# Kernel tuning notes

Measured on AMD Instinct MI355X. Metric: run time of the kernel, lower is better.

## Reference

```python
import jax, jax.numpy as jnp
import numpy as np

N = 50000
E = 1600000
IN_C = 128
HID = 128
OUT_C = 64


def setup_inputs() -> dict:
    key = jax.random.key(0)
    ks = jax.random.split(key, 10)
    x = jax.random.normal(ks[0], (N, IN_C), dtype=jnp.float32)
    edge_index = jax.random.randint(ks[1], (2, E), 0, N, dtype=jnp.int64)
    s = lambda fan_in: 1.0 / np.sqrt(fan_in)
    W1 = jax.random.uniform(ks[2], (HID, IN_C), jnp.float32, -s(IN_C), s(IN_C))
    b1 = jnp.zeros((HID,), jnp.float32)
    Wc = jax.random.uniform(ks[3], (HID, HID + IN_C), jnp.float32, -s(HID + IN_C), s(HID + IN_C))
    bc = jax.random.uniform(ks[4], (HID,), jnp.float32, -s(HID + IN_C), s(HID + IN_C))
    W2 = jax.random.uniform(ks[5], (HID, HID), jnp.float32, -s(HID), s(HID))
    b2 = jnp.zeros((HID,), jnp.float32)
    Wo = jax.random.uniform(ks[6], (OUT_C, 2 * HID), jnp.float32, -s(2 * HID), s(2 * HID))
    bo = jax.random.uniform(ks[7], (OUT_C,), jnp.float32, -s(2 * HID), s(2 * HID))
    return {"x": x, "edge_index": edge_index, "W1": W1, "b1": b1,
            "Wc": Wc, "bc": bc, "W2": W2, "b2": b2, "Wo": Wo, "bo": bo}


def _gcn_conv(x, src, dst, norm, W, b):
    # PyG GCNConv: h = x @ W^T, propagate with sym-norm coeffs, add bias.
    h = x @ W.T                                   # [N, F_out]
    msg = h[src] * norm[:, None]                  # gather + scale, [E+N, F_out]
    out = jax.ops.segment_sum(msg, dst, num_segments=N)  # scatter-add
    return out + b


def _norm_coeffs(edge_index):
    # add self-loops, then sym normalization: D^{-1/2} A_hat D^{-1/2}
    loop = jnp.arange(N, dtype=edge_index.dtype)
    src = jnp.concatenate([edge_index[0], loop])
    dst = jnp.concatenate([edge_index[1], loop])
    deg = jax.ops.segment_sum(jnp.ones_like(dst, dtype=jnp.float32), dst, num_segments=N)
    dis = jnp.where(deg > 0, jax.lax.rsqrt(deg), 0.0)
    norm = dis[src] * dis[dst]
    return src, dst, norm


def reference(x, edge_index, W1, b1, Wc, bc, W2, b2, Wo, bo):
    src, dst, norm = _norm_coeffs(edge_index)
    x_agg = jax.nn.relu(_gcn_conv(x, src, dst, norm, W1, b1))
    x_comb = jnp.concatenate([x_agg, x], axis=1)
    x_comb = jax.nn.relu(x_comb @ Wc.T + bc)
    # dropout is identity in eval mode
    x_agg2 = _gcn_conv(x_comb, src, dst, norm, W2, b2)
    x_out = jnp.concatenate([x_agg2, x_comb], axis=1)
    return x_out @ Wo.T + bo
```

## Files before the change

kernel.cpp:

```cpp
#include <hip/hip_runtime.h>
#include <hip/hip_fp16.h>

#define Nn 50000
#define Ee 1600000
#define NPART 8

typedef __attribute__((ext_vector_type(8))) short short8;
typedef __attribute__((ext_vector_type(4))) float f32x4;
typedef unsigned short ushort;
typedef unsigned int uint;

__device__ __forceinline__ ushort f32_to_bf16(float f) {
    unsigned u = __builtin_bit_cast(unsigned, f);
    unsigned r = u + 0x7FFFu + ((u >> 16) & 1u);
    return (ushort)(r >> 16);
}
__device__ __forceinline__ float bf16_to_f32(ushort h) {
    unsigned u = ((unsigned)h) << 16;
    return __builtin_bit_cast(float, u);
}


__global__ void hist_rank_kernel(const int* __restrict__ dst, int* __restrict__ counts8,
                                 int* __restrict__ rank) {
    int e = blockIdx.x * blockDim.x + threadIdx.x;
    int p = blockIdx.x & (NPART - 1);
    if (e < Ee) rank[e] = atomicAdd(&counts8[p * Nn + dst[e]], 1);
}

__global__ void scan1_kernel(const int* __restrict__ counts8, int* __restrict__ offsets,
                             int* __restrict__ partials) {
    __shared__ int sd[256];
    int t = threadIdx.x;
    int i = blockIdx.x * 256 + t;
    int c = 0;
    if (i < Nn) {
        #pragma unroll
        for (int p = 0; p < NPART; ++p) c += counts8[p * Nn + i];
    }
    int v = c;
    #pragma unroll
    for (int off = 1; off < 256; off <<= 1) {
        sd[t] = v; __syncthreads();
        int add = (t >= off) ? sd[t - off] : 0;
        __syncthreads();
        v += add;
    }
    if (i < Nn) offsets[i] = v - c;
    if (t == 255) partials[blockIdx.x] = v;
}

__global__ void scan3_kernel(int* __restrict__ offsets, const int* __restrict__ partials,
                             const int* __restrict__ counts8, int* __restrict__ pbase8,
                             float* __restrict__ dis) {
    __shared__ int sd[256];
    int t = threadIdx.x;
    int s = (t < blockIdx.x) ? partials[t] : 0;
    sd[t] = s; __syncthreads();
    #pragma unroll
    for (int off = 128; off > 0; off >>= 1) {
        if (t < off) sd[t] += sd[t + off];
        __syncthreads();
    }
    int base = sd[0];
    int i = blockIdx.x * 256 + t;
    if (i == 0) offsets[Nn] = Ee;
    if (i < Nn) {
        int off = offsets[i] + base;
        offsets[i] = off;
        int running = off;
        #pragma unroll
        for (int p = 0; p < NPART; ++p) {
            pbase8[p * Nn + i] = running;
            running += counts8[p * Nn + i];
        }
        dis[i] = rsqrtf((float)(running - off + 1));
    }
}

__global__ void fill_csr_rank(const int* __restrict__ ei, const int* __restrict__ rank,
                              const int* __restrict__ pbase8, int* __restrict__ csr) {
    int e = blockIdx.x * blockDim.x + threadIdx.x;
    int p = blockIdx.x & (NPART - 1);
    if (e < Ee) {
        int d = ei[Ee + e];
        csr[pbase8[p * Nn + d] + rank[e]] = ei[e];
    }
}

__global__ void prep_w_kernel(const float* __restrict__ W1, const float* __restrict__ Wc,
                              const float* __restrict__ W2, const float* __restrict__ Wo,
                              ushort* __restrict__ base) {
    int i = blockIdx.x * 256 + threadIdx.x;
    const float* src; ushort* hi; ushort* lo; int idx;
    if (i < 16384)      { src = W1; hi = base;          lo = base + 16384;  idx = i; }
    else if (i < 49152) { src = Wc; hi = base + 32768;  lo = base + 65536;  idx = i - 16384; }
    else if (i < 65536) { src = W2; hi = base + 98304;  lo = base + 114688; idx = i - 49152; }
    else                { src = Wo; hi = base + 131072; lo = base + 147456; idx = i - 65536; }
    float f = src[idx];
    ushort hb = f32_to_bf16(f);
    hi[idx] = hb;
    lo[idx] = f32_to_bf16(f - bf16_to_f32(hb));
}

__global__ void split_x_kernel(const float* __restrict__ x, ushort* __restrict__ xhi,
                               ushort* __restrict__ xlo) {
    int i = (blockIdx.x * 256 + threadIdx.x) * 4;
    float4 v = *(const float4*)(x + i);
    float vv[4] = {v.x, v.y, v.z, v.w};
    ushort h[4], l[4];
    #pragma unroll
    for (int j = 0; j < 4; ++j) {
        h[j] = f32_to_bf16(vv[j]);
        l[j] = f32_to_bf16(vv[j] - bf16_to_f32(h[j]));
    }
    *(uint2*)(xhi + i) = make_uint2((uint)h[0] | ((uint)h[1] << 16),
                                    (uint)h[2] | ((uint)h[3] << 16));
    *(uint2*)(xlo + i) = make_uint2((uint)l[0] | ((uint)l[1] << 16),
                                    (uint)l[2] | ((uint)l[3] << 16));
}

template <int CO, int K, bool RELU, bool HASBIAS, bool SCALEDIS, int OUTMODE>
__global__ __launch_bounds__(256, 3) void mfma_gemm(
    const ushort* __restrict__ AH0, const ushort* __restrict__ AL0,
    const ushort* __restrict__ AH1, const ushort* __restrict__ AL1,
    const ushort* __restrict__ Whi, const ushort* __restrict__ Wlo,
    const float* __restrict__ bias, const float* __restrict__ dis,
    void* __restrict__ outp, ushort* __restrict__ outLo) {
    constexpr int NF = CO / 16;
    constexpr int NCH = K / 64;
    constexpr int WISS = CO / 32;

    __shared__ ushort lds[2 * 64 * 64 + 2 * CO * 64];
    ushort* ldsAh = lds;
    ushort* ldsAl = lds + 64 * 64;
    ushort* ldsWh = lds + 2 * 64 * 64;
    ushort* ldsWl = ldsWh + CO * 64;

    int tid  = threadIdx.x;
    int wave = tid >> 6;
    int lane = tid & 63;
    int c = lane & 15;
    int g = lane >> 4;
    int row0 = blockIdx.x * 64;

    f32x4 acc1[NF], acc2[NF];
    #pragma unroll
    for (int f = 0; f < NF; ++f) {
        acc1[f] = (f32x4){0.f, 0.f, 0.f, 0.f};
        acc2[f] = (f32x4){0.f, 0.f, 0.f, 0.f};
    }

    #pragma unroll
    for (int ch = 0; ch < NCH; ++ch) {
        const int k0 = ch * 64;
        const ushort* Ah = (K == 256 && k0 >= 128) ? AH1 : AH0;
        const ushort* Al = (K == 256 && k0 >= 128) ? AL1 : AL0;
        const int kb = (K == 256 && k0 >= 128) ? (k0 - 128) : k0;

        #pragma unroll
        for (int i = 0; i < 2; ++i) {
            int idx = tid + i * 256;
            int row = idx >> 3, kg = idx & 7;
            int gr = row0 + row; gr = (gr < Nn) ? gr : (Nn - 1);
            int sb = (kg * 16) ^ ((row & 7) << 4);
            int ldsoff = (i * 256 + wave * 64) * 8;
            __builtin_amdgcn_global_load_lds(Ah + (size_t)gr * 128 + kb + (sb >> 1),
                                             &ldsAh[ldsoff], 16, 0, 0);
            __builtin_amdgcn_global_load_lds(Al + (size_t)gr * 128 + kb + (sb >> 1),
                                             &ldsAl[ldsoff], 16, 0, 0);
        }
        #pragma unroll
        for (int i = 0; i < WISS; ++i) {
            int idx = tid + i * 256;
            int col = idx >> 3, kg = idx & 7;
            int sb = (kg * 16) ^ ((col & 7) << 4);
            int ldsoff = (i * 256 + wave * 64) * 8;
            __builtin_amdgcn_global_load_lds(Whi + (size_t)col * K + k0 + (sb >> 1),
                                             &ldsWh[ldsoff], 16, 0, 0);
            __builtin_amdgcn_global_load_lds(Wlo + (size_t)col * K + k0 + (sb >> 1),
                                             &ldsWl[ldsoff], 16, 0, 0);
        }
        __syncthreads();

        #pragma unroll
        for (int s = 0; s < 2; ++s) {
            int arow = wave * 16 + c;
            int ab = (s * 64 + g * 16) ^ ((arow & 7) << 4);
            short8 ahi = *(const short8*)((const char*)ldsAh + arow * 128 + ab);
            short8 alo = *(const short8*)((const char*)ldsAl + arow * 128 + ab);
            #pragma unroll
            for (int f = 0; f < NF; ++f) {
                int col = f * 16 + c;
                int wb = (s * 64 + g * 16) ^ ((col & 7) << 4);
                short8 bh = *(const short8*)((const char*)ldsWh + col * 128 + wb);
                short8 bl = *(const short8*)((const char*)ldsWl + col * 128 + wb);
                acc1[f] = __builtin_amdgcn_mfma_f32_16x16x32_bf16(ahi, bh, acc1[f], 0, 0, 0);
                acc2[f] = __builtin_amdgcn_mfma_f32_16x16x32_bf16(ahi, bl, acc2[f], 0, 0, 0);
                acc2[f] = __builtin_amdgcn_mfma_f32_16x16x32_bf16(alo, bh, acc2[f], 0, 0, 0);
            }
        }
        __syncthreads();
    }

    #pragma unroll
    for (int f = 0; f < NF; ++f) {
        int col = f * 16 + c;
        float bv = HASBIAS ? bias[col] : 0.f;
        #pragma unroll
        for (int rg = 0; rg < 4; ++rg) {
            int row = row0 + wave * 16 + g * 4 + rg;
            if (row < Nn) {
                float v = acc1[f][rg] + acc2[f][rg] + bv;
                if (RELU) v = fmaxf(v, 0.f);
                if (SCALEDIS) v *= dis[row];
                size_t idx = (size_t)row * CO + col;
                if constexpr (OUTMODE == 1) {
                    ((__half*)outp)[idx] = __float2half_rn(v);
                } else if constexpr (OUTMODE == 2) {
                    ushort hb = f32_to_bf16(v);
                    ((ushort*)outp)[idx] = hb;
                    outLo[idx] = f32_to_bf16(v - bf16_to_f32(hb));
                } else {
                    ((float*)outp)[idx] = v;
                }
            }
        }
    }
}

template <bool RELU>
__global__ __launch_bounds__(256) void propagate_kernel(
    const __half* __restrict__ gbuf, const int* __restrict__ offs,
    const int* __restrict__ csr, const float* __restrict__ dis,
    const float* __restrict__ bias, ushort* __restrict__ outHi,
    ushort* __restrict__ outLo) {
    int node = blockIdx.x * 4 + (threadIdx.x >> 6);
    if (node >= Nn) return;
    int lane = threadIdx.x & 63;
    float2 sv = __half22float2(*((const __half2*)(gbuf + ((size_t)node << 7)) + lane));
    float ax = sv.x, ay = sv.y;
    int beg = offs[node], end = offs[node + 1];
    int e = beg;
    for (; e + 8 <= end; e += 8) {
        int s0 = csr[e],     s1 = csr[e + 1], s2 = csr[e + 2], s3 = csr[e + 3];
        int s4 = csr[e + 4], s5 = csr[e + 5], s6 = csr[e + 6], s7 = csr[e + 7];
        __half2 h0 = *((const __half2*)(gbuf + ((size_t)s0 << 7)) + lane);
        __half2 h1 = *((const __half2*)(gbuf + ((size_t)s1 << 7)) + lane);
        __half2 h2 = *((const __half2*)(gbuf + ((size_t)s2 << 7)) + lane);
        __half2 h3 = *((const __half2*)(gbuf + ((size_t)s3 << 7)) + lane);
        __half2 h4 = *((const __half2*)(gbuf + ((size_t)s4 << 7)) + lane);
        __half2 h5 = *((const __half2*)(gbuf + ((size_t)s5 << 7)) + lane);
        __half2 h6 = *((const __half2*)(gbuf + ((size_t)s6 << 7)) + lane);
        __half2 h7 = *((const __half2*)(gbuf + ((size_t)s7 << 7)) + lane);
        float2 v0 = __half22float2(h0), v1 = __half22float2(h1);
        float2 v2 = __half22float2(h2), v3 = __half22float2(h3);
        float2 v4 = __half22float2(h4), v5 = __half22float2(h5);
        float2 v6 = __half22float2(h6), v7 = __half22float2(h7);
        ax += ((v0.x + v1.x) + (v2.x + v3.x)) + ((v4.x + v5.x) + (v6.x + v7.x));
        ay += ((v0.y + v1.y) + (v2.y + v3.y)) + ((v4.y + v5.y) + (v6.y + v7.y));
    }
    for (; e < end; ++e) {
        int s = csr[e];
        float2 v = __half22float2(*((const __half2*)(gbuf + ((size_t)s << 7)) + lane));
        ax += v.x;
        ay += v.y;
    }
    float di = dis[node];
    ax = fmaf(di, ax, bias[lane * 2]);
    ay = fmaf(di, ay, bias[lane * 2 + 1]);
    if (RELU) { ax = fmaxf(ax, 0.f); ay = fmaxf(ay, 0.f); }
    ushort hx = f32_to_bf16(ax), hy = f32_to_bf16(ay);
    ushort lx = f32_to_bf16(ax - bf16_to_f32(hx));
    ushort ly = f32_to_bf16(ay - bf16_to_f32(hy));
    ((uint*)(outHi + ((size_t)node << 7)))[lane] = (uint)hx | ((uint)hy << 16);
    ((uint*)(outLo + ((size_t)node << 7)))[lane] = (uint)lx | ((uint)ly << 16);
}


extern "C" void kernel_launch(void* const* d_in, const int* in_sizes, int n_in,
                              void* d_out, int out_size, void* d_ws, size_t ws_size,
                              hipStream_t stream) {
    const float* x  = (const float*)d_in[0];
    const int*   ei = (const int*)d_in[1];
    const float* W1 = (const float*)d_in[2];
    const float* b1 = (const float*)d_in[3];
    const float* Wc = (const float*)d_in[4];
    const float* bc = (const float*)d_in[5];
    const float* W2 = (const float*)d_in[6];
    const float* b2 = (const float*)d_in[7];
    const float* Wo = (const float*)d_in[8];
    const float* bo = (const float*)d_in[9];
    float* out = (float*)d_out;

    char* base = (char*)d_ws;
    auto carve = [&](size_t bytes) {
        void* p = (void*)base;
        base += (bytes + 255) & ~(size_t)255;
        return p;
    };
    char*  tmp      = (char*)carve(4 * 1024 * 1024);
    int*   counts8  = (int*)tmp;
    int*   pbase8   = (int*)(tmp + 2 * 1024 * 1024);
    ushort* wplanes = (ushort*)tmp;
    int*   offsets  = (int*)carve((Nn + 1) * sizeof(int));
    int*   partials = (int*)carve(256 * sizeof(int));
    float* dis      = (float*)carve(Nn * sizeof(float));
    int*   rank     = (int*)carve((size_t)Ee * sizeof(int));
    int*   csr      = (int*)carve((size_t)Ee * sizeof(int));
    __half* gbuf    = (__half*)carve((size_t)Nn * 128 * sizeof(__half));
    ushort* xhi     = (ushort*)carve((size_t)Nn * 128 * sizeof(ushort));
    ushort* xlo     = (ushort*)carve((size_t)Nn * 128 * sizeof(ushort));
    ushort* aggHi   = (ushort*)carve((size_t)Nn * 128 * sizeof(ushort));
    ushort* aggLo   = (ushort*)carve((size_t)Nn * 128 * sizeof(ushort));
    ushort* combHi  = (ushort*)carve((size_t)Nn * 128 * sizeof(ushort));
    ushort* combLo  = (ushort*)carve((size_t)Nn * 128 * sizeof(ushort));

    const ushort* w1hi = wplanes;
    const ushort* w1lo = wplanes + 16384;
    const ushort* wchi = wplanes + 32768;
    const ushort* wclo = wplanes + 65536;
    const ushort* w2hi = wplanes + 98304;
    const ushort* w2lo = wplanes + 114688;
    const ushort* wohi = wplanes + 131072;
    const ushort* wolo = wplanes + 147456;

    const int SCAN_BLOCKS = (Nn + 255) / 256;
    const int EB = (Ee + 255) / 256;

    hipMemsetAsync(counts8, 0, NPART * Nn * sizeof(int), stream);
    hist_rank_kernel<<<EB, 256, 0, stream>>>(ei + Ee, counts8, rank);
    scan1_kernel<<<SCAN_BLOCKS, 256, 0, stream>>>(counts8, offsets, partials);
    scan3_kernel<<<SCAN_BLOCKS, 256, 0, stream>>>(offsets, partials, counts8, pbase8, dis);
    fill_csr_rank<<<EB, 256, 0, stream>>>(ei, rank, pbase8, csr);

    prep_w_kernel<<<320, 256, 0, stream>>>(W1, Wc, W2, Wo, (ushort*)wplanes);
    split_x_kernel<<<6250, 256, 0, stream>>>(x, xhi, xlo);

    const int GB = (Nn + 63) / 64;
    const int PB = (Nn + 3) / 4;

    mfma_gemm<128, 128, false, false, true, 1><<<GB, 256, 0, stream>>>(
        xhi, xlo, nullptr, nullptr, w1hi, w1lo, nullptr, dis, gbuf, nullptr);
    propagate_kernel<true><<<PB, 256, 0, stream>>>(gbuf, offsets, csr, dis, b1, aggHi, aggLo);
    mfma_gemm<128, 256, true, true, false, 2><<<GB, 256, 0, stream>>>(
        aggHi, aggLo, xhi, xlo, wchi, wclo, bc, nullptr, combHi, combLo);
    mfma_gemm<128, 128, false, false, true, 1><<<GB, 256, 0, stream>>>(
        combHi, combLo, nullptr, nullptr, w2hi, w2lo, nullptr, dis, gbuf, nullptr);
    propagate_kernel<false><<<PB, 256, 0, stream>>>(gbuf, offsets, csr, dis, b2, aggHi, aggLo);
    mfma_gemm<64, 256, false, true, false, 0><<<GB, 256, 0, stream>>>(
        aggHi, aggLo, combHi, combLo, wohi, wolo, bo, nullptr, out, nullptr);
}
```

Measured before the change: 376.3 us.

## Pad CSR rows to multiples of eight and pick histogram partition by XCC id

Each node's CSR row is padded to a multiple of 8 with dummy source indices that point at a zeroed extra gbuf row, so the propagate loop needs no scalar tail. The histogram partition is now chosen from the hardware XCC id read via s_getreg instead of block index, and the partition is packed into the rank so fill_csr can recover it. The aim is to keep atomics local to one XCC's cache and to remove divergent tail iterations, at the cost of extra padded gathers and a serial padding loop in the scan.

```diff
diff --git a/kernel.cpp b/kernel.cpp
--- a/kernel.cpp
+++ b/kernel.cpp
@@ -4,6 +4,7 @@
 #define Nn 50000
 #define Ee 1600000
 #define NPART 8
+#define XCC_GETREG_IMM 6164
 
 typedef __attribute__((ext_vector_type(8))) short short8;
 typedef __attribute__((ext_vector_type(4))) float f32x4;
@@ -24,8 +25,11 @@
 __global__ void hist_rank_kernel(const int* __restrict__ dst, int* __restrict__ counts8,
                                  int* __restrict__ rank) {
     int e = blockIdx.x * blockDim.x + threadIdx.x;
-    int p = blockIdx.x & (NPART - 1);
-    if (e < Ee) rank[e] = atomicAdd(&counts8[p * Nn + dst[e]], 1);
+    int p = __builtin_amdgcn_s_getreg(XCC_GETREG_IMM) & (NPART - 1);
+    if (e < Ee) {
+        int r = atomicAdd(&counts8[p * Nn + dst[e]], 1);
+        rank[e] = r | (p << 28);
+    }
 }
 
 __global__ void scan1_kernel(const int* __restrict__ counts8, int* __restrict__ offsets,
@@ -33,12 +37,14 @@
     __shared__ int sd[256];
     int t = threadIdx.x;
     int i = blockIdx.x * 256 + t;
-    int c = 0;
+    int cp = 0;
     if (i < Nn) {
+        int c = 0;
         #pragma unroll
         for (int p = 0; p < NPART; ++p) c += counts8[p * Nn + i];
-    }
-    int v = c;
+        cp = (c + 7) & ~7;
+    }
+    int v = cp;
     #pragma unroll
     for (int off = 1; off < 256; off <<= 1) {
         sd[t] = v; __syncthreads();
@@ -46,13 +52,13 @@
         __syncthreads();
         v += add;
     }
-    if (i < Nn) offsets[i] = v - c;
+    if (i < Nn) offsets[i] = v - cp;
     if (t == 255) partials[blockIdx.x] = v;
 }
 
 __global__ void scan3_kernel(int* __restrict__ offsets, const int* __restrict__ partials,
                              const int* __restrict__ counts8, int* __restrict__ pbase8,
-                             float* __restrict__ dis) {
+                             float* __restrict__ dis, int* __restrict__ csr) {
     __shared__ int sd[256];
     int t = threadIdx.x;
     int s = (t < blockIdx.x) ? partials[t] : 0;
@@ -64,7 +70,6 @@
     }
     int base = sd[0];
     int i = blockIdx.x * 256 + t;
-    if (i == 0) offsets[Nn] = Ee;
     if (i < Nn) {
         int off = offsets[i] + base;
         offsets[i] = off;
@@ -74,17 +79,23 @@
             pbase8[p * Nn + i] = running;
             running += counts8[p * Nn + i];
         }
-        dis[i] = rsqrtf((float)(running - off + 1));
+        int deg = running - off;
+        int cp  = (deg + 7) & ~7;
+        for (int j = running; j < off + cp; ++j) csr[j] = Nn;
+        dis[i] = rsqrtf((float)(deg + 1));
+        if (i == Nn - 1) offsets[Nn] = off + cp;
     }
 }
 
 __global__ void fill_csr_rank(const int* __restrict__ ei, const int* __restrict__ rank,
                               const int* __restrict__ pbase8, int* __restrict__ csr) {
     int e = blockIdx.x * blockDim.x + threadIdx.x;
-    int p = blockIdx.x & (NPART - 1);
     if (e < Ee) {
         int d = ei[Ee + e];
-        csr[pbase8[p * Nn + d] + rank[e]] = ei[e];
+        int rk = rank[e];
+        int p = (rk >> 28) & (NPART - 1);
+        int r = rk & 0x0FFFFFFF;
+        csr[pbase8[p * Nn + d] + r] = ei[e];
     }
 }
 
@@ -241,8 +252,7 @@
     float2 sv = __half22float2(*((const __half2*)(gbuf + ((size_t)node << 7)) + lane));
     float ax = sv.x, ay = sv.y;
     int beg = offs[node], end = offs[node + 1];
-    int e = beg;
-    for (; e + 8 <= end; e += 8) {
+    for (int e = beg; e < end; e += 8) {
         int s0 = csr[e],     s1 = csr[e + 1], s2 = csr[e + 2], s3 = csr[e + 3];
         int s4 = csr[e + 4], s5 = csr[e + 5], s6 = csr[e + 6], s7 = csr[e + 7];
         __half2 h0 = *((const __half2*)(gbuf + ((size_t)s0 << 7)) + lane);
@@ -260,12 +270,6 @@
         ax += ((v0.x + v1.x) + (v2.x + v3.x)) + ((v4.x + v5.x) + (v6.x + v7.x));
         ay += ((v0.y + v1.y) + (v2.y + v3.y)) + ((v4.y + v5.y) + (v6.y + v7.y));
     }
-    for (; e < end; ++e) {
-        int s = csr[e];
-        float2 v = __half22float2(*((const __half2*)(gbuf + ((size_t)s << 7)) + lane));
-        ax += v.x;
-        ay += v.y;
-    }
     float di = dis[node];
     ax = fmaf(di, ax, bias[lane * 2]);
     ay = fmaf(di, ay, bias[lane * 2 + 1]);
@@ -307,8 +311,8 @@
     int*   partials = (int*)carve(256 * sizeof(int));
     float* dis      = (float*)carve(Nn * sizeof(float));
     int*   rank     = (int*)carve((size_t)Ee * sizeof(int));
-    int*   csr      = (int*)carve((size_t)Ee * sizeof(int));
-    __half* gbuf    = (__half*)carve((size_t)Nn * 128 * sizeof(__half));
+    int*   csr      = (int*)carve(((size_t)Ee + 8 * Nn) * sizeof(int));
+    __half* gbuf    = (__half*)carve((size_t)(Nn + 2) * 128 * sizeof(__half));
     ushort* xhi     = (ushort*)carve((size_t)Nn * 128 * sizeof(ushort));
     ushort* xlo     = (ushort*)carve((size_t)Nn * 128 * sizeof(ushort));
     ushort* aggHi   = (ushort*)carve((size_t)Nn * 128 * sizeof(ushort));
@@ -329,9 +333,10 @@
     const int EB = (Ee + 255) / 256;
 
     hipMemsetAsync(counts8, 0, NPART * Nn * sizeof(int), stream);
+    hipMemsetAsync(gbuf + (size_t)Nn * 128, 0, 256, stream);
     hist_rank_kernel<<<EB, 256, 0, stream>>>(ei + Ee, counts8, rank);
     scan1_kernel<<<SCAN_BLOCKS, 256, 0, stream>>>(counts8, offsets, partials);
-    scan3_kernel<<<SCAN_BLOCKS, 256, 0, stream>>>(offsets, partials, counts8, pbase8, dis);
+    scan3_kernel<<<SCAN_BLOCKS, 256, 0, stream>>>(offsets, partials, counts8, pbase8, dis, csr);
     fill_csr_rank<<<EB, 256, 0, stream>>>(ei, rank, pbase8, csr);
 
     prep_w_kernel<<<320, 256, 0, stream>>>(W1, Wc, W2, Wo, (ushort*)wplanes);
```

Measured after the change: 373.3 us. Within noise of the previous version (-0.8%).
